# Performance work log

Hardware: AMD Instinct MI355X
Metric: run time of the kernel (lower is better)

The kernel has to match this reference:

```python
import jax, jax.numpy as jnp
import numpy as np

NUM_INTERNAL = 4000
MAX_CHILDREN = 16
BATCH = 1024


def _build_tree():
    # Deterministic synthetic hierarchy: child counts in [2, 16].
    counts = 2 + (np.arange(NUM_INTERNAL) * 7) % 15
    row = np.repeat(np.arange(NUM_INTERNAL), counts)
    col = np.concatenate([np.arange(n) for n in counts])
    flat_index = row * MAX_CHILDREN + col          # scatter slots in padded buffer
    num_nodes = int(counts.sum()) + 1              # +1 for the root
    child_index = np.arange(1, num_nodes)          # every non-root node is a child once
    return flat_index, child_index, num_nodes


def setup_inputs() -> dict:
    flat_index, child_index, num_nodes = _build_tree()
    key = jax.random.key(0)
    scores = jax.random.normal(key, (BATCH, flat_index.shape[0]), dtype=jnp.float32)
    return {
        "scores": scores,
        "flat_index": jnp.asarray(flat_index, dtype=jnp.int32),
        "child_index": jnp.asarray(child_index, dtype=jnp.int32),
        "num_internal": NUM_INTERNAL,
        "max_num_children": MAX_CHILDREN,
        "num_nodes": num_nodes,
    }


def reference(scores, flat_index, child_index, num_internal, max_num_children, num_nodes):
    lead = scores.shape[:-1]
    neg_inf = jnp.asarray(-jnp.inf, scores.dtype)
    # Scatter scores into padded [num_internal, max_num_children] buffer (-inf padding).
    flat = jnp.full((*lead, num_internal * max_num_children), neg_inf, dtype=scores.dtype)
    flat = flat.at[..., flat_index].set(scores)
    # Per-internal-node (grouped) log-softmax over the padded child axis.
    child_log_p = jax.nn.log_softmax(
        flat.reshape(*lead, num_internal, max_num_children), axis=-1
    ).reshape(*lead, num_internal * max_num_children)
    # Gather real slots back and scatter into node-indexed output (root stays 0).
    out = jnp.zeros((*lead, num_nodes), dtype=scores.dtype)
    out = out.at[..., child_index].set(child_log_p[..., flat_index])
    return out


if __name__ == "__main__":
    inp = setup_inputs()
    y = reference(**inp)
    print(y.shape, y.dtype)
```

## Files before the change

kernel.cpp:

```cpp
#include <hip/hip_runtime.h>
#include <math.h>

#define MAXC 16
#define GPB  256
#define BLOCK 256
#define LBUF_SZ (GPB * MAXC + 32)

__global__ void build_meta_kernel(const int* __restrict__ flat_index,
                                  const int* __restrict__ p_num_internal,
                                  const int* __restrict__ p_max_children,
                                  int n_scores,
                                  int* __restrict__ offs,
                                  unsigned short* __restrict__ gid16) {
    int j = blockIdx.x * blockDim.x + threadIdx.x;
    int mc = p_max_children[0];
    if (j < n_scores) {
        int fi = flat_index[j];
        int g  = fi / mc;
        gid16[j] = (unsigned short)g;
        if (fi - g * mc == 0) offs[g] = j;
    }
    if (j == 0) offs[p_num_internal[0]] = n_scores;
}

__global__ void __launch_bounds__(BLOCK)
hier_logsoftmax_kernel(const float* __restrict__ scores,
                       const int* __restrict__ offs,
                       const unsigned short* __restrict__ gid16,
                       const int* __restrict__ p_num_internal,
                       float* __restrict__ out,
                       int n_scores, int num_nodes) {
    __shared__ __align__(16) float lbuf[LBUF_SZ];
    __shared__ float lse[GPB];

    const int ni = p_num_internal[0];
    const int nchunks = (ni + GPB - 1) / GPB;
    const int b = blockIdx.y;
    const float* __restrict__ srow = scores + (size_t)b * (size_t)n_scores;
    float* __restrict__ orow = out + (size_t)b * (size_t)num_nodes;

    for (int chunk = blockIdx.x; chunk < nchunks; chunk += gridDim.x) {
        const int g0   = chunk * GPB;
        const int gend = min(g0 + GPB, ni);
        const int e0   = offs[g0];
        const int e1   = offs[gend];
        const int n    = e1 - e0;
        const int d    = e0 & 3;

        {
            const int hL  = min(n, (4 - (e0 & 3)) & 3);
            const int nvL = (n - hL) >> 2;
            for (int q = threadIdx.x; q < nvL; q += BLOCK) {
                const int i = hL + 4 * q;
                const float4 t = *(const float4*)&srow[e0 + i];
                *(float4*)&lbuf[d + i] = t;
            }
            for (int i = hL + 4 * nvL + threadIdx.x; i < n; i += BLOCK)
                lbuf[d + i] = srow[e0 + i];
            if (threadIdx.x < hL) lbuf[d + threadIdx.x] = srow[e0 + threadIdx.x];
        }
        __syncthreads();

        {
            const int g = g0 + threadIdx.x;
            if (g < gend) {
                const int og = offs[g];
                const int lo = d + (og - e0);
                const int c  = offs[g + 1] - og;
                float v[MAXC];
                #pragma unroll
                for (int k = 0; k < MAXC; ++k)
                    v[k] = (k < c) ? lbuf[lo + k] : -INFINITY;
                float m = v[0];
                #pragma unroll
                for (int k = 1; k < MAXC; ++k) m = fmaxf(m, v[k]);
                float s = 0.0f;
                #pragma unroll
                for (int k = 0; k < MAXC; ++k) s += __expf(v[k] - m);
                lse[threadIdx.x] = m + __logf(s);
            }
        }
        __syncthreads();

        {
            const unsigned short* __restrict__ grow = gid16 + e0;
            const int hS  = min(n, (4 - ((1 + e0) & 3)) & 3);
            const int nvS = (n - hS) >> 2;
            for (int q = threadIdx.x; q < nvS; q += BLOCK) {
                const int i = hS + 4 * q;
                float4 t;
                t.x = lbuf[d + i]     - lse[grow[i]     - g0];
                t.y = lbuf[d + i + 1] - lse[grow[i + 1] - g0];
                t.z = lbuf[d + i + 2] - lse[grow[i + 2] - g0];
                t.w = lbuf[d + i + 3] - lse[grow[i + 3] - g0];
                *(float4*)&orow[1 + e0 + i] = t;
            }
            for (int i = hS + 4 * nvS + threadIdx.x; i < n; i += BLOCK)
                orow[1 + e0 + i] = lbuf[d + i] - lse[grow[i] - g0];
            if (threadIdx.x < hS)
                orow[1 + e0 + threadIdx.x] = lbuf[d + threadIdx.x] - lse[grow[threadIdx.x] - g0];
        }
        if (chunk == 0 && threadIdx.x == 0) orow[0] = 0.0f;
        __syncthreads();
    }
}

extern "C" void kernel_launch(void* const* d_in, const int* in_sizes, int n_in,
                              void* d_out, int out_size, void* d_ws, size_t ws_size,
                              hipStream_t stream) {
    const float* scores     = (const float*)d_in[0];
    const int*   flat_index = (const int*)d_in[1];
    const int*   p_ni       = (const int*)d_in[3];
    const int*   p_mc       = (const int*)d_in[4];

    const int n_scores  = in_sizes[1];
    const int batch     = in_sizes[0] / n_scores;
    const int num_nodes = out_size / batch;

    int* offs = (int*)d_ws;
    unsigned short* gid16 = (unsigned short*)((char*)d_ws + ((size_t)(n_scores + 2) * 4 + 255 & ~(size_t)255));
    float* out = (float*)d_out;

    {
        dim3 blk(256), grd((n_scores + 255) / 256);
        hipLaunchKernelGGL(build_meta_kernel, grd, blk, 0, stream,
                           flat_index, p_ni, p_mc, n_scores, offs, gid16);
    }

    {
        dim3 blk(BLOCK), grd(16, batch);
        hipLaunchKernelGGL(hier_logsoftmax_kernel, grd, blk, 0, stream,
                           scores, offs, gid16, p_ni, out, n_scores, num_nodes);
    }
}
```

Baseline: 272.0 us.

## Process multiple batch rows per block with register prefetch and in-place LDS normalization

Each block now handles 8 batch rows for a chunk of groups. It reuses the per-thread group metadata across those rows and prefetches the next row's scores into registers while the current row is computed. The group's log-softmax is written in place into LDS, which removes the gid16 lookup array and the lse table during the store phase. Stores read shifted float4 values from LDS, and barriers use a custom s_waitcnt plus s_barrier sequence. The cost is fewer blocks, higher register pressure, and a fixed LDS capacity (CAP) that assumes a chunk holds at most about 2464 elements.

```diff
diff --git a/kernel.cpp b/kernel.cpp
--- a/kernel.cpp
+++ b/kernel.cpp
@@ -1,72 +1,110 @@
 #include <hip/hip_runtime.h>
 #include <math.h>
 
-#define MAXC 16
-#define GPB  256
+#define MAXC  16
+#define GPB   256
 #define BLOCK 256
-#define LBUF_SZ (GPB * MAXC + 32)
+#define ROWS  8
+#define CAP   2464
 
-__global__ void build_meta_kernel(const int* __restrict__ flat_index,
+__global__ void build_offs_kernel(const int* __restrict__ flat_index,
                                   const int* __restrict__ p_num_internal,
                                   const int* __restrict__ p_max_children,
                                   int n_scores,
-                                  int* __restrict__ offs,
-                                  unsigned short* __restrict__ gid16) {
+                                  int* __restrict__ offs) {
     int j = blockIdx.x * blockDim.x + threadIdx.x;
     int mc = p_max_children[0];
     if (j < n_scores) {
         int fi = flat_index[j];
         int g  = fi / mc;
-        gid16[j] = (unsigned short)g;
         if (fi - g * mc == 0) offs[g] = j;
     }
     if (j == 0) offs[p_num_internal[0]] = n_scores;
 }
 
+__device__ __forceinline__ void bar_lds() {
+    asm volatile("s_waitcnt lgkmcnt(0)" ::: "memory");
+    __builtin_amdgcn_s_barrier();
+    asm volatile("" ::: "memory");
+}
+
 __global__ void __launch_bounds__(BLOCK)
 hier_logsoftmax_kernel(const float* __restrict__ scores,
                        const int* __restrict__ offs,
-                       const unsigned short* __restrict__ gid16,
                        const int* __restrict__ p_num_internal,
                        float* __restrict__ out,
-                       int n_scores, int num_nodes) {
-    __shared__ __align__(16) float lbuf[LBUF_SZ];
-    __shared__ float lse[GPB];
+                       int n_scores, int num_nodes, int batch) {
+    __shared__ __align__(16) float lbuf[CAP];
+    __shared__ float dump[BLOCK];
 
-    const int ni = p_num_internal[0];
+    const int ni      = p_num_internal[0];
     const int nchunks = (ni + GPB - 1) / GPB;
-    const int b = blockIdx.y;
-    const float* __restrict__ srow = scores + (size_t)b * (size_t)n_scores;
-    float* __restrict__ orow = out + (size_t)b * (size_t)num_nodes;
+    const int tid     = (int)threadIdx.x;
+    const int b0      = (int)blockIdx.y * ROWS;
+    if (b0 >= batch) return;
+    const int nrows = min(ROWS, batch - b0);
 
-    for (int chunk = blockIdx.x; chunk < nchunks; chunk += gridDim.x) {
+    for (int chunk = (int)blockIdx.x; chunk < nchunks; chunk += (int)gridDim.x) {
         const int g0   = chunk * GPB;
         const int gend = min(g0 + GPB, ni);
         const int e0   = offs[g0];
-        const int e1   = offs[gend];
-        const int n    = e1 - e0;
+        const int n    = offs[gend] - e0;
         const int d    = e0 & 3;
 
-        {
-            const int hL  = min(n, (4 - (e0 & 3)) & 3);
-            const int nvL = (n - hL) >> 2;
-            for (int q = threadIdx.x; q < nvL; q += BLOCK) {
-                const int i = hL + 4 * q;
-                const float4 t = *(const float4*)&srow[e0 + i];
-                *(float4*)&lbuf[d + i] = t;
+        const int hL  = min(n, (4 - (e0 & 3)) & 3);
+        const int nvL = (n - hL) >> 2;
+        const int tL  = n - hL - 4 * nvL;
+
+        const int A0  = 1 + e0;
+        const int hS  = min(n, (4 - (A0 & 3)) & 3);
+        const int nvS = (n - hS) >> 2;
+        const int tS  = n - hS - 4 * nvS;
+        const int B0  = (d + hS) >> 2;
+
+        const int g = g0 + tid;
+        int lo = 0, c = 0;
+        if (g < gend) {
+            const int og = offs[g];
+            c  = offs[g + 1] - og;
+            lo = d + (og - e0);
+        }
+
+        const int  i0 = hL + 4 * tid;
+        const int  i1 = i0 + 4 * BLOCK;
+        const int  i2 = i1 + 4 * BLOCK;
+        const bool q0 = tid < nvL, q1 = tid + BLOCK < nvL, q2 = tid + 2 * BLOCK < nvL;
+        const int  it = hL + 4 * nvL + tid;
+        const bool qh = tid < hL, qt = tid < tL;
+
+        const float* sr = scores + (size_t)b0 * n_scores + e0;
+        float4 r0, r1, r2;
+        float  rh = 0.f, rt = 0.f;
+        if (q0) r0 = *(const float4*)(sr + i0);
+        if (q1) r1 = *(const float4*)(sr + i1);
+        if (q2) r2 = *(const float4*)(sr + i2);
+        if (qh) rh = sr[tid];
+        if (qt) rt = sr[it];
+
+        for (int rr = 0; rr < nrows; ++rr) {
+            float* __restrict__ orow = out + (size_t)(b0 + rr) * num_nodes;
+
+            if (q0) *(float4*)&lbuf[d + i0] = r0;
+            if (q1) *(float4*)&lbuf[d + i1] = r1;
+            if (q2) *(float4*)&lbuf[d + i2] = r2;
+            if (qh) lbuf[d + tid] = rh;
+            if (qt) lbuf[d + it]  = rt;
+            bar_lds();
+
+            if (rr + 1 < nrows) {
+                const float* s2 = scores + (size_t)(b0 + rr + 1) * n_scores + e0;
+                if (q0) r0 = *(const float4*)(s2 + i0);
+                if (q1) r1 = *(const float4*)(s2 + i1);
+                if (q2) r2 = *(const float4*)(s2 + i2);
+                if (qh) rh = s2[tid];
+                if (qt) rt = s2[it];
             }
-            for (int i = hL + 4 * nvL + threadIdx.x; i < n; i += BLOCK)
-                lbuf[d + i] = srow[e0 + i];
-            if (threadIdx.x < hL) lbuf[d + threadIdx.x] = srow[e0 + threadIdx.x];
-        }
-        __syncthreads();
 
-        {
-            const int g = g0 + threadIdx.x;
             if (g < gend) {
-                const int og = offs[g];
-                const int lo = d + (og - e0);
-                const int c  = offs[g + 1] - og;
                 float v[MAXC];
                 #pragma unroll
                 for (int k = 0; k < MAXC; ++k)
@@ -74,34 +112,35 @@
                 float m = v[0];
                 #pragma unroll
                 for (int k = 1; k < MAXC; ++k) m = fmaxf(m, v[k]);
-                float s = 0.0f;
+                float s0 = 0.f, s1 = 0.f;
                 #pragma unroll
-                for (int k = 0; k < MAXC; ++k) s += __expf(v[k] - m);
-                lse[threadIdx.x] = m + __logf(s);
+                for (int k = 0; k < MAXC; k += 2) {
+                    s0 += __expf(v[k] - m);
+                    s1 += __expf(v[k + 1] - m);
+                }
+                const float lse = m + __logf(s0 + s1);
+                #pragma unroll
+                for (int k = 0; k < MAXC; ++k) {
+                    float* p = (k < c) ? &lbuf[lo + k] : &dump[tid];
+                    *p = v[k] - lse;
+                }
             }
+            bar_lds();
+
+            for (int p = tid; p < nvS; p += BLOCK) {
+                const float  x   = lbuf[4 * (B0 + p) + 3];
+                const float4 blk = *(const float4*)&lbuf[4 * (B0 + p + 1)];
+                float4 t; t.x = x; t.y = blk.x; t.z = blk.y; t.w = blk.z;
+                *(float4*)&orow[A0 + hS + 4 * p] = t;
+            }
+            if (tid < hS) orow[A0 + tid] = lbuf[d + tid];
+            if (tid < tS) {
+                const int j = hS + 4 * nvS + tid;
+                orow[A0 + j] = lbuf[d + j];
+            }
+            if (chunk == 0 && tid == 0) orow[0] = 0.0f;
+            bar_lds();
         }
-        __syncthreads();
-
-        {
-            const unsigned short* __restrict__ grow = gid16 + e0;
-            const int hS  = min(n, (4 - ((1 + e0) & 3)) & 3);
-            const int nvS = (n - hS) >> 2;
-            for (int q = threadIdx.x; q < nvS; q += BLOCK) {
-                const int i = hS + 4 * q;
-                float4 t;
-                t.x = lbuf[d + i]     - lse[grow[i]     - g0];
-                t.y = lbuf[d + i + 1] - lse[grow[i + 1] - g0];
-                t.z = lbuf[d + i + 2] - lse[grow[i + 2] - g0];
-                t.w = lbuf[d + i + 3] - lse[grow[i + 3] - g0];
-                *(float4*)&orow[1 + e0 + i] = t;
-            }
-            for (int i = hS + 4 * nvS + threadIdx.x; i < n; i += BLOCK)
-                orow[1 + e0 + i] = lbuf[d + i] - lse[grow[i] - g0];
-            if (threadIdx.x < hS)
-                orow[1 + e0 + threadIdx.x] = lbuf[d + threadIdx.x] - lse[grow[threadIdx.x] - g0];
-        }
-        if (chunk == 0 && threadIdx.x == 0) orow[0] = 0.0f;
-        __syncthreads();
     }
 }
 
@@ -118,18 +157,17 @@
     const int num_nodes = out_size / batch;
 
     int* offs = (int*)d_ws;
-    unsigned short* gid16 = (unsigned short*)((char*)d_ws + ((size_t)(n_scores + 2) * 4 + 255 & ~(size_t)255));
-    float* out = (float*)d_out;
 
     {
         dim3 blk(256), grd((n_scores + 255) / 256);
-        hipLaunchKernelGGL(build_meta_kernel, grd, blk, 0, stream,
-                           flat_index, p_ni, p_mc, n_scores, offs, gid16);
+        hipLaunchKernelGGL(build_offs_kernel, grd, blk, 0, stream,
+                           flat_index, p_ni, p_mc, n_scores, offs);
     }
 
     {
-        dim3 blk(BLOCK), grd(16, batch);
+        dim3 blk(BLOCK), grd(16, (batch + ROWS - 1) / ROWS);
         hipLaunchKernelGGL(hier_logsoftmax_kernel, grd, blk, 0, stream,
-                           scores, offs, gid16, p_ni, out, n_scores, num_nodes);
+                           scores, offs, p_ni, out_size ? (float*)d_out : (float*)d_out,
+                           n_scores, num_nodes, batch);
     }
 }
```

After: 276.1 us. Within noise of the previous version (+1.5%).
